# Optimization experiments

Hardware: AMD Instinct MI355X
Metric: run time of the kernel (lower is better)

## Reference

```python
import jax, jax.numpy as jnp
import numpy as np

RAY_START, RAY_END = 2.25, 3.3
DEPTH_RES, N_IMPORTANCE = 48, 48
BOX_WARP = 1.0
PLANE_AXES = jnp.array([[[1.,0.,0.],[0.,1.,0.],[0.,0.,1.]],
                        [[1.,0.,0.],[0.,0.,1.],[0.,1.,0.]],
                        [[0.,0.,1.],[1.,0.,0.],[0.,1.,0.]]], jnp.float32)


def grid_sample_bilinear(feat, gx, gy):
    # feat [B,C,H,W]; gx,gy [B,M] in [-1,1]; bilinear, zeros padding, align_corners=False
    B, C, H, W = feat.shape
    x = (gx + 1.0) * (W * 0.5) - 0.5
    y = (gy + 1.0) * (H * 0.5) - 0.5
    x0 = jnp.floor(x); y0 = jnp.floor(y)
    wx = (x - x0)[:, None, :]; wy = (y - y0)[:, None, :]
    x0i = x0.astype(jnp.int32); y0i = y0.astype(jnp.int32)
    flat = feat.reshape(B, C, H * W)
    def gather(xi, yi):
        valid = ((xi >= 0) & (xi < W) & (yi >= 0) & (yi < H)).astype(feat.dtype)
        idx = jnp.clip(yi, 0, H - 1) * W + jnp.clip(xi, 0, W - 1)
        v = jnp.take_along_axis(flat, jnp.broadcast_to(idx[:, None, :], (B, C, idx.shape[-1])), axis=2)
        return v * valid[:, None, :]
    v00 = gather(x0i, y0i); v10 = gather(x0i + 1, y0i)
    v01 = gather(x0i, y0i + 1); v11 = gather(x0i + 1, y0i + 1)
    return (v00 * (1 - wx) * (1 - wy) + v10 * wx * (1 - wy)
            + v01 * (1 - wx) * wy + v11 * wx * wy)  # [B,C,M]


def sample_from_planes(planes_feat, coords):
    # planes_feat [N,3,C,H,W], coords [N,M,3] -> [N,3,M,C]
    N, P, C, H, W = planes_feat.shape
    M = coords.shape[1]
    c = (2.0 / BOX_WARP) * coords
    inv = jnp.linalg.inv(PLANE_AXES)  # [P,3,3]
    proj = jnp.einsum('nmi,pij->npmj', c, inv)[..., :2]
    out = grid_sample_bilinear(planes_feat.reshape(N * P, C, H, W),
                               proj[..., 0].reshape(N * P, M),
                               proj[..., 1].reshape(N * P, M))
    return out.reshape(N, P, C, M).transpose(0, 1, 3, 2)


def decode(feats, w1, b1, w2, b2):
    # OSGDecoder: mean over planes, Linear->softplus->Linear
    x = feats.mean(axis=1)
    h = jax.nn.softplus(x @ w1 + b1)
    o = h @ w2 + b2
    sigma = o[..., :1]
    rgb = jax.nn.sigmoid(o[..., 1:]) * (1 + 2 * 0.001) - 0.001
    return rgb, sigma


def ray_march(colors, densities, depths, color_bg=None):
    # MipRayMarcher2 with softplus density clamp and BG compositing via final transmittance
    deltas = depths[:, :, 1:] - depths[:, :, :-1]
    colors_mid = 0.5 * (colors[:, :, :-1] + colors[:, :, 1:])
    densities_mid = jax.nn.softplus(0.5 * (densities[:, :, :-1] + densities[:, :, 1:]) - 1.0)
    depths_mid = 0.5 * (depths[:, :, :-1] + depths[:, :, 1:])
    alpha = 1.0 - jnp.exp(-densities_mid * deltas)
    alpha_shifted = jnp.concatenate([jnp.ones_like(alpha[:, :, :1]), 1 - alpha + 1e-10], axis=2)
    T = jnp.cumprod(alpha_shifted, axis=2)
    weights = alpha * T[:, :, :-1]
    comp_rgb = (weights * colors_mid).sum(axis=2)
    weight_total = weights.sum(axis=2)
    comp_depth = jnp.nan_to_num((weights * depths_mid).sum(axis=2) / weight_total, nan=float('inf'))
    comp_depth = jnp.clip(comp_depth, depths.min(), depths.max())
    bg_trans = T[:, :, -1]  # [B,R,1]
    if color_bg is not None:
        comp_rgb = comp_rgb + bg_trans * color_bg
    comp_rgb = comp_rgb * 2.0 - 1.0
    return comp_rgb, comp_depth, weights, alpha, bg_trans


def sample_pdf(bins, weights, n_importance, eps=1e-5):
    # inverse-CDF importance sampling (deterministic midpoint u)
    nw = weights.shape[-1]
    weights = weights + eps
    pdf = weights / weights.sum(axis=-1, keepdims=True)
    cdf = jnp.concatenate([jnp.zeros_like(pdf[:, :1]), jnp.cumsum(pdf, axis=-1)], axis=-1)
    u = (jnp.arange(n_importance, dtype=cdf.dtype) + 0.5) / n_importance
    u = jnp.broadcast_to(u, (cdf.shape[0], n_importance))
    inds = jax.vmap(lambda c, uu: jnp.searchsorted(c, uu, side='right'))(cdf, u)
    below = jnp.clip(inds - 1, 0, nw)
    above = jnp.clip(inds, 0, nw)
    cdf_b = jnp.take_along_axis(cdf, below, axis=-1)
    cdf_a = jnp.take_along_axis(cdf, above, axis=-1)
    bins_b = jnp.take_along_axis(bins, below, axis=-1)
    bins_a = jnp.take_along_axis(bins, above, axis=-1)
    denom = jnp.where(cdf_a - cdf_b < eps, 1.0, cdf_a - cdf_b)
    return bins_b + (u - cdf_b) / denom * (bins_a - bins_b)


def sample_importance(z_vals, weights, n_importance):
    B, R, S, _ = z_vals.shape
    z = z_vals.reshape(B * R, S)
    w = weights.reshape(B * R, -1) + 0.01
    wp = jnp.pad(w, ((0, 0), (1, 1)), constant_values=-np.inf)
    w = jnp.maximum(wp[:, :-1], wp[:, 1:])      # max_pool1d(k=2,s=1,p=1)
    w = 0.5 * (w[:, :-1] + w[:, 1:]) + 0.01     # avg_pool1d(k=2,s=1)
    z_mid = 0.5 * (z[:, :-1] + z[:, 1:])
    z_fine = sample_pdf(z_mid, w[:, 1:-1], n_importance)
    return jax.lax.stop_gradient(z_fine).reshape(B, R, n_importance, 1)


def unify_samples(d1, c1, s1, d2, c2, s2):
    depths = jnp.concatenate([d1, d2], axis=2)
    colors = jnp.concatenate([c1, c2], axis=2)
    dens = jnp.concatenate([s1, s2], axis=2)
    idx = jnp.argsort(depths, axis=2)
    depths = jnp.take_along_axis(depths, idx, axis=2)
    colors = jnp.take_along_axis(colors, jnp.broadcast_to(idx, colors.shape), axis=2)
    dens = jnp.take_along_axis(dens, idx, axis=2)
    return depths, colors, dens


def sample_stratified(B, R, dtype):
    S = DEPTH_RES
    delta = (RAY_END - RAY_START) / (S - 1)
    d = jnp.linspace(RAY_START, RAY_END, S, dtype=dtype).reshape(1, 1, S, 1) + 0.5 * delta
    return jnp.broadcast_to(d, (B, R, S, 1))


def setup_inputs() -> dict:
    key = jax.random.key(0)
    ks = jax.random.split(key, 10)
    B, R, C, H = 4, 4096, 32, 256
    planes = 0.1 * jax.random.normal(ks[0], (B, 3, C, H, H), jnp.float32)
    ray_origins = jnp.array([0.0, 0.0, 2.7]) + 0.03 * jax.random.normal(ks[1], (B, R, 3), jnp.float32)
    uv = jax.random.uniform(ks[2], (B, R, 2), jnp.float32, -0.4, 0.4)
    d = jnp.concatenate([uv, -jnp.ones((B, R, 1), jnp.float32)], axis=-1)
    ray_directions = d / jnp.linalg.norm(d, axis=-1, keepdims=True)
    z_bg = jax.random.normal(ks[3], (B, 64), jnp.float32)
    dec_w1 = jax.random.normal(ks[4], (C, 64), jnp.float32) / np.sqrt(C)
    dec_b1 = jnp.zeros((64,), jnp.float32)
    dec_w2 = jax.random.normal(ks[5], (64, 33), jnp.float32) / 8.0
    dec_b2 = jnp.zeros((33,), jnp.float32)
    bg_w1 = jax.random.normal(ks[6], (67, 64), jnp.float32) / np.sqrt(67)
    bg_b1 = jnp.zeros((64,), jnp.float32)
    bg_w2 = jax.random.normal(ks[7], (64, 32), jnp.float32) / 8.0
    bg_b2 = jnp.zeros((32,), jnp.float32)
    return dict(planes=planes, ray_origins=ray_origins, ray_directions=ray_directions, z_bg=z_bg,
                dec_w1=dec_w1, dec_b1=dec_b1, dec_w2=dec_w2, dec_b2=dec_b2,
                bg_w1=bg_w1, bg_b1=bg_b1, bg_w2=bg_w2, bg_b2=bg_b2)


def reference(planes, ray_origins, ray_directions, z_bg, dec_w1, dec_b1, dec_w2, dec_b2,
              bg_w1, bg_b1, bg_w2, bg_b2):
    B, R, _ = ray_origins.shape
    S = DEPTH_RES
    depths_coarse = sample_stratified(B, R, planes.dtype)
    coords = (ray_origins[:, :, None, :] + depths_coarse * ray_directions[:, :, None, :]).reshape(B, -1, 3)
    feats = sample_from_planes(planes, coords)
    rgb_c, sig_c = decode(feats, dec_w1, dec_b1, dec_w2, dec_b2)
    rgb_c = rgb_c.reshape(B, R, S, -1)
    sig_c = sig_c.reshape(B, R, S, 1)
    # Ball background feature: MLP on [dir, z_bg]
    z = jnp.broadcast_to(z_bg[:, None, :], (B, R, z_bg.shape[-1]))
    hb = jax.nn.softplus(jnp.concatenate([ray_directions, z], axis=-1) @ bg_w1 + bg_b1)
    color_bg = jax.nn.sigmoid(hb @ bg_w2 + bg_b2)  # [B,R,32]
    _, _, w_coarse, _, _ = ray_march(rgb_c, sig_c, depths_coarse)
    depths_fine = sample_importance(depths_coarse, w_coarse, N_IMPORTANCE)
    coords_f = (ray_origins[:, :, None, :] + depths_fine * ray_directions[:, :, None, :]).reshape(B, -1, 3)
    feats_f = sample_from_planes(planes, coords_f)
    rgb_f, sig_f = decode(feats_f, dec_w1, dec_b1, dec_w2, dec_b2)
    rgb_f = rgb_f.reshape(B, R, N_IMPORTANCE, -1)
    sig_f = sig_f.reshape(B, R, N_IMPORTANCE, 1)
    depths_all, rgb_all, sig_all = unify_samples(depths_coarse, rgb_c, sig_c, depths_fine, rgb_f, sig_f)
    rgb_final, depth_final, weights, alpha, bg_T = ray_march(rgb_all, sig_all, depths_all, color_bg)
    return rgb_final, depth_final, weights.sum(axis=2)
```

## Files before the change

### kernel.cpp

```cpp
#include <hip/hip_runtime.h>
#include <hip/hip_bf16.h>
#include <math.h>

#define NB 4
#define NR 4096
#define NC 32
#define NH 256
#define NW 256
#define NS 48
#define NRAYS (NB*NR)
#define NSAMP (NRAYS*NS)

__device__ __forceinline__ float coarse_depth(int i) {
    const float DELTA = 1.05f / 47.f;
    return 2.25f + i * DELTA + 0.5f * DELTA;
}
__device__ __forceinline__ float zmid_c(int i) {
    return 0.5f * (coarse_depth(i) + coarse_depth(i + 1));
}
__device__ __forceinline__ float softplus_f(float x) {
    return fmaxf(x, 0.f) + __logf(1.f + __expf(-fabsf(x)));
}
__device__ __forceinline__ float sigmoid_f(float x) {
    return __frcp_rn(1.f + __expf(-x));
}

__global__ __launch_bounds__(256) void k_transpose(const float* __restrict__ in,
                                                   float* __restrict__ out) {
    __shared__ float tile[32][65];
    int bp = blockIdx.x >> 10;
    int t0 = (blockIdx.x & 1023) * 64;
    const float* src = in + (size_t)bp * NC * NH * NW;
    float* dst = out + (size_t)bp * NH * NW * NC;
    int px = threadIdx.x & 63;
    int c0 = threadIdx.x >> 6;
    #pragma unroll
    for (int cc = 0; cc < 32; cc += 4)
        tile[cc + c0][px] = src[(size_t)(cc + c0) * NH * NW + t0 + px];
    __syncthreads();
    int c = threadIdx.x & 31;
    int p0 = threadIdx.x >> 5;
    #pragma unroll
    for (int pp = 0; pp < 64; pp += 8)
        dst[(size_t)(t0 + pp + p0) * NC + c] = tile[c][pp + p0];
}

__global__ __launch_bounds__(64) void k_const(const float* __restrict__ b1,
                                              const float* __restrict__ w2,
                                              const float* __restrict__ b2,
                                              float* __restrict__ const_o) {
    __shared__ float h[64];
    int j = threadIdx.x;
    h[j] = softplus_f(b1[j]);
    __syncthreads();
    if (j < 33) {
        float o = b2[j];
        #pragma unroll 1
        for (int i = 0; i < 64; ++i) o += h[i] * w2[i * 33 + j];
        const_o[j] = (j == 0) ? o : sigmoid_f(o) * 1.002f - 0.001f;
    }
}

template<bool FINE>
__global__ __launch_bounds__(256) void k_sample_decode(
    const float* __restrict__ planes_t,
    const float* __restrict__ origins,
    const float* __restrict__ dirs,
    const float* __restrict__ dfine,
    const float* __restrict__ w1, const float* __restrict__ b1,
    const float* __restrict__ w2, const float* __restrict__ b2,
    const float* __restrict__ const_o,
    float* __restrict__ rgb_out, float* __restrict__ sig_out)
{
    __shared__ float xbuf[256][33];
    __shared__ float w1t[64][32];
    __shared__ float w2p[64][36];
    __shared__ float b1s[64];
    __shared__ float b2s[36];
    __shared__ float cbuf[36];

    for (int i = threadIdx.x; i < 2048; i += 256) {
        int j = i >> 5, c = i & 31;
        w1t[j][c] = w1[c * 64 + j];
    }
    for (int i = threadIdx.x; i < 64 * 36; i += 256) {
        int j = i / 36, kx = i - j * 36;
        w2p[j][kx] = (kx < 33) ? w2[j * 33 + kx] : 0.f;
    }
    if (threadIdx.x < 64) b1s[threadIdx.x] = b1[threadIdx.x];
    if (threadIdx.x < 36) {
        b2s[threadIdx.x]  = (threadIdx.x < 33) ? b2[threadIdx.x] : 0.f;
        cbuf[threadIdx.x] = (threadIdx.x < 33) ? const_o[threadIdx.x] : 0.f;
    }

    int lane  = threadIdx.x & 63;
    int wbase = threadIdx.x & 192;
    int s0    = blockIdx.x * 256 + wbase;

    int s   = s0 + lane;
    int ray = s / NS;
    int kk  = s - ray * NS;
    float t = FINE ? dfine[s] : coarse_depth(kk);
    float ox = origins[ray*3+0], oy = origins[ray*3+1], oz = origins[ray*3+2];
    float ddx = dirs[ray*3+0],   ddy = dirs[ray*3+1],   ddz = dirs[ray*3+2];
    float cx = 2.f * (ox + t * ddx);
    float cy = 2.f * (oy + t * ddy);
    float cz = 2.f * (oz + t * ddz);
    int bi = ray >> 12;
    int   m_base[3];
    float m_q[3][4];
    #pragma unroll
    for (int p = 0; p < 3; ++p) {
        float gx = (p == 2) ? cz : cx;
        float gy = (p == 0) ? cy : ((p == 1) ? cz : cx);
        float fx = (gx + 1.f) * 128.f - 0.5f;
        float fy = (gy + 1.f) * 128.f - 0.5f;
        float x0f = floorf(fx), y0f = floorf(fy);
        float wx = fx - x0f, wy = fy - y0f;
        int x0 = (int)x0f, y0 = (int)y0f;
        if (x0 >= -1 && x0 <= 255 && y0 >= -1 && y0 <= 255) {
            float wxm = 1.f - wx, wym = 1.f - wy;
            float q00 = wxm*wym, q10 = wx*wym, q01 = wxm*wy, q11 = wx*wy;
            if (!(x0 >= 0   && y0 >= 0))   q00 = 0.f;
            if (!(x0 <= 254 && y0 >= 0))   q10 = 0.f;
            if (!(x0 >= 0   && y0 <= 254)) q01 = 0.f;
            if (!(x0 <= 254 && y0 <= 254)) q11 = 0.f;
            m_base[p] = (bi*3 + p) * (NH*NW*NC) + (y0*NW + x0)*NC;
            m_q[p][0] = q00; m_q[p][1] = q10; m_q[p][2] = q01; m_q[p][3] = q11;
        } else {
            m_base[p] = -1;
            m_q[p][0] = m_q[p][1] = m_q[p][2] = m_q[p][3] = 0.f;
        }
    }

    int ch   = lane & 31;
    int half = lane >> 5;
    #pragma unroll 1
    for (int i = 0; i < 64; i += 2) {
        int src = i + half;
        float acc = 0.f;
        #pragma unroll
        for (int p = 0; p < 3; ++p) {
            int   bse = __shfl(m_base[p], src);
            float q00 = __shfl(m_q[p][0], src);
            float q10 = __shfl(m_q[p][1], src);
            float q01 = __shfl(m_q[p][2], src);
            float q11 = __shfl(m_q[p][3], src);
            if (bse >= 0) {
                const float* ptr = planes_t + (size_t)bse + ch;
                acc += q00 * ptr[0]    + q10 * ptr[32]
                     + q01 * ptr[8192] + q11 * ptr[8224];
            }
        }
        xbuf[wbase + i + half][ch] = acc * (1.f / 3.f);
    }
    __syncthreads();

    bool empty = (m_base[0] < 0) & (m_base[1] < 0) & (m_base[2] < 0);
    float sig;
    if (!empty) {
        float x[32];
        #pragma unroll
        for (int c = 0; c < 32; ++c) x[c] = xbuf[threadIdx.x][c];
        float o[36];
        #pragma unroll
        for (int k2 = 0; k2 < 36; ++k2) o[k2] = b2s[k2];
        #pragma unroll 1
        for (int j = 0; j < 64; ++j) {
            float a = b1s[j];
            #pragma unroll
            for (int c = 0; c < 32; ++c) a += x[c] * w1t[j][c];
            float h = softplus_f(a);
            #pragma unroll
            for (int k2 = 0; k2 < 36; ++k2) o[k2] += h * w2p[j][k2];
        }
        sig = o[0];
        #pragma unroll
        for (int c = 0; c < 32; ++c)
            xbuf[threadIdx.x][c] = sigmoid_f(o[1 + c]) * 1.002f - 0.001f;
    } else {
        sig = cbuf[0];
        #pragma unroll
        for (int c = 0; c < 32; ++c) xbuf[threadIdx.x][c] = cbuf[1 + c];
    }
    sig_out[s] = sig;
    __syncthreads();

    #pragma unroll 1
    for (int i = 0; i < 64; i += 2) {
        int r = wbase + i + half;
        rgb_out[(size_t)(blockIdx.x * 256 + r) * 32 + ch] = xbuf[r][ch];
    }
}

__global__ __launch_bounds__(256) void k_importance(const float* __restrict__ sig,
                                                    float* __restrict__ dfine) {
    int ray = blockIdx.x * 256 + threadIdx.x;
    const float* sp = sig + (size_t)ray * NS;
    float w[47];
    float T = 1.f;
    float sprev = sp[0];
    #pragma unroll
    for (int i = 0; i < 47; ++i) {
        float scur = sp[i + 1];
        float dens = softplus_f(0.5f * (sprev + scur) - 1.f);
        float delta = coarse_depth(i + 1) - coarse_depth(i);
        float alpha = 1.f - __expf(-dens * delta);
        w[i] = alpha * T + 0.01f;
        T *= (1.f - alpha + 1e-10f);
        sprev = scur;
    }
    float p[45];
    float sum = 0.f;
    #pragma unroll
    for (int i = 1; i <= 45; ++i) {
        float nwi  = fmaxf(w[i - 1], w[i]);
        float nwi1 = fmaxf(w[i], w[i + 1]);
        float wb = 0.5f * (nwi + nwi1) + 0.01f;
        float v = wb + 1e-5f;
        p[i - 1] = v;
        sum += v;
    }
    int k = 0;
    float cdf_lo = 0.f;
    #pragma unroll
    for (int i = 0; i < 45; ++i) {
        float cdf_hi = cdf_lo + p[i] / sum;
        float bb = zmid_c(i), ba = zmid_c(i + 1);
        float denom = cdf_hi - cdf_lo;
        if (denom < 1e-5f) denom = 1.f;
        while (k < 48) {
            float u = (k + 0.5f) / 48.f;
            if (u < cdf_hi) {
                dfine[(size_t)ray * NS + k] = bb + (u - cdf_lo) / denom * (ba - bb);
                ++k;
            } else break;
        }
        cdf_lo = cdf_hi;
    }
    while (k < 48) {
        dfine[(size_t)ray * NS + k] = zmid_c(45);
        ++k;
    }
}

__global__ __launch_bounds__(256) void k_final(
    const float* __restrict__ sig_c, const float* __restrict__ rgb_c,
    const float* __restrict__ sig_f, const float* __restrict__ rgb_f,
    const float* __restrict__ dfine,
    const float* __restrict__ dirs, const float* __restrict__ z_bg,
    const float* __restrict__ bw1, const float* __restrict__ bb1,
    const float* __restrict__ bw2, const float* __restrict__ bb2,
    float* __restrict__ out_rgb, float* __restrict__ out_dep,
    float* __restrict__ out_wt)
{
    __shared__ float s_d[4][96];
    __shared__ float s_sig[4][96];
    __shared__ int   s_src[4][96];
    __shared__ float s_fine[4][48];
    __shared__ float s_w[4][96];
    __shared__ float s_g[4][96];
    __shared__ float s_h[4][64];
    __shared__ float s_zb[64];
    int lane = threadIdx.x & 63;
    int wv = threadIdx.x >> 6;
    int ray = blockIdx.x * 4 + wv;
    int bi = (blockIdx.x * 4) >> 12;
    if (threadIdx.x < 64) s_zb[threadIdx.x] = z_bg[bi * 64 + threadIdx.x];
    if (lane < 48) s_fine[wv][lane] = dfine[(size_t)ray * NS + lane];
    __syncthreads();

    if (lane < 48) {
        float cd = coarse_depth(lane);
        int lo = 0, hi = 48;
        while (lo < hi) { int mid = (lo + hi) >> 1;
            if (s_fine[wv][mid] < cd) lo = mid + 1; else hi = mid; }
        int rc = lane + lo;
        s_d[wv][rc] = cd;
        s_sig[wv][rc] = sig_c[(size_t)ray * NS + lane];
        s_src[wv][rc] = lane;
        float f = s_fine[wv][lane];
        lo = 0; hi = 48;
        while (lo < hi) { int mid = (lo + hi) >> 1;
            if (coarse_depth(mid) <= f) lo = mid + 1; else hi = mid; }
        int rf = lane + lo;
        s_d[wv][rf] = f;
        s_sig[wv][rf] = sig_f[(size_t)ray * NS + lane];
        s_src[wv][rf] = 48 + lane;
    }
    float ddx = dirs[ray*3+0], ddy = dirs[ray*3+1], ddz = dirs[ray*3+2];
    __syncthreads();

    float alpha0 = 0.f, alpha1 = 0.f, a0 = 1.f, a1 = 1.f;
    float dm0 = 0.f, dm1 = 0.f;
    if (lane < 48) {
        int i0 = 2 * lane, i1 = i0 + 1;
        float d0 = s_d[wv][i0], sA = s_sig[wv][i0];
        float d1 = s_d[wv][i1], sB = s_sig[wv][i1];
        {
            float dens = softplus_f(0.5f * (sA + sB) - 1.f);
            alpha0 = 1.f - __expf(-dens * (d1 - d0));
            a0 = 1.f - alpha0 + 1e-10f;
            dm0 = 0.5f * (d0 + d1);
        }
        if (i1 < 95) {
            float d2 = s_d[wv][i1 + 1], sC = s_sig[wv][i1 + 1];
            float dens = softplus_f(0.5f * (sB + sC) - 1.f);
            alpha1 = 1.f - __expf(-dens * (d2 - d1));
            a1 = 1.f - alpha1 + 1e-10f;
            dm1 = 0.5f * (d1 + d2);
        }
    }
    float P = a0 * a1;
    #pragma unroll
    for (int off = 1; off < 64; off <<= 1) {
        float t = __shfl_up(P, off);
        if (lane >= off) P *= t;
    }
    float T_all = __shfl(P, 63);
    float E = __shfl_up(P, 1);
    if (lane == 0) E = 1.f;
    float w0 = alpha0 * E;
    float w1 = alpha1 * (E * a0);
    float sw = w0 + w1;
    float sd = w0 * dm0 + w1 * dm1;
    #pragma unroll
    for (int off = 32; off; off >>= 1) {
        sw += __shfl_xor(sw, off);
        sd += __shfl_xor(sd, off);
    }
    if (lane < 48) {
        s_w[wv][2 * lane] = w0;
        s_w[wv][2 * lane + 1] = w1;
    }
    __syncthreads();
    {
        int i = lane;
        float wm = (i > 0) ? s_w[wv][i - 1] : 0.f;
        s_g[wv][i] = 0.5f * (wm + s_w[wv][i]);
        int i2 = lane + 64;
        if (lane < 32)
            s_g[wv][i2] = 0.5f * (s_w[wv][i2 - 1] + s_w[wv][i2]);
    }

    float a = bb1[lane] + ddx * bw1[lane] + ddy * bw1[64 + lane] + ddz * bw1[128 + lane];
    #pragma unroll 1
    for (int i = 0; i < 64; ++i) a += s_zb[i] * bw1[(3 + i) * 64 + lane];
    s_h[wv][lane] = softplus_f(a);
    __syncthreads();
    int c = lane & 31;
    float ob = bb2[c];
    #pragma unroll 1
    for (int j = 0; j < 64; ++j) ob += s_h[wv][j] * bw2[j * 32 + c];
    float bgc = sigmoid_f(ob);

    int h = lane >> 5;
    size_t rbase = (size_t)ray * NS * 32;
    const float* b0p = rgb_c + rbase;
    const float* b1p = rgb_f + rbase - (size_t)48 * 32;
    float acc = 0.f;
    #pragma unroll 4
    for (int i = h; i < 96; i += 2) {
        int src = s_src[wv][i];
        const float* cp = ((src < 48) ? b0p : b1p) + (size_t)src * 32;
        acc += s_g[wv][i] * cp[c];
    }
    acc += __shfl_xor(acc, 32);

    float rgbv = (acc + T_all * bgc) * 2.f - 1.f;
    float dep = sd / sw;
    if (!(dep == dep)) dep = INFINITY;
    dep = fminf(fmaxf(dep, coarse_depth(0)), coarse_depth(47));
    if (lane < 32) out_rgb[(size_t)ray * 32 + c] = rgbv;
    if (lane == 0) { out_dep[ray] = dep; out_wt[ray] = sw; }
}

extern "C" void kernel_launch(void* const* d_in, const int* in_sizes, int n_in,
                              void* d_out, int out_size, void* d_ws, size_t ws_size,
                              hipStream_t stream) {
    (void)in_sizes; (void)n_in; (void)out_size; (void)ws_size;
    const float* planes  = (const float*)d_in[0];
    const float* origins = (const float*)d_in[1];
    const float* dirs    = (const float*)d_in[2];
    const float* z_bg    = (const float*)d_in[3];
    const float* dw1     = (const float*)d_in[4];
    const float* db1     = (const float*)d_in[5];
    const float* dw2     = (const float*)d_in[6];
    const float* db2     = (const float*)d_in[7];
    const float* bw1     = (const float*)d_in[8];
    const float* bb1     = (const float*)d_in[9];
    const float* bw2     = (const float*)d_in[10];
    const float* bb2     = (const float*)d_in[11];

    char* ws = (char*)d_ws;
    size_t off = 0;
    float* sig_c    = (float*)(ws + off); off += (size_t)NSAMP * 4;
    float* sig_f    = (float*)(ws + off); off += (size_t)NSAMP * 4;
    float* dfine    = (float*)(ws + off); off += (size_t)NSAMP * 4;
    float* const_o  = (float*)(ws + off); off += 4096;
    float* planes_t = (float*)(ws + off); off += (size_t)NB * 3 * NH * NW * NC * 4;
    float* rgb_c    = (float*)(ws + off); off += (size_t)NSAMP * 32 * 4;
    float* rgb_f    = (float*)(ws + off); off += (size_t)NSAMP * 32 * 4;

    float* out_rgb = (float*)d_out;
    float* out_dep = out_rgb + (size_t)NRAYS * 32;
    float* out_wt  = out_dep + NRAYS;

    k_const<<<dim3(1), dim3(64), 0, stream>>>(db1, dw2, db2, const_o);
    k_transpose<<<dim3(NB * 3 * 1024), dim3(256), 0, stream>>>(planes, planes_t);
    k_sample_decode<false><<<dim3(NSAMP / 256), dim3(256), 0, stream>>>(
        planes_t, origins, dirs, (const float*)nullptr,
        dw1, db1, dw2, db2, const_o, rgb_c, sig_c);
    k_importance<<<dim3(NRAYS / 256), dim3(256), 0, stream>>>(sig_c, dfine);
    k_sample_decode<true><<<dim3(NSAMP / 256), dim3(256), 0, stream>>>(
        planes_t, origins, dirs, dfine,
        dw1, db1, dw2, db2, const_o, rgb_f, sig_f);
    k_final<<<dim3(NRAYS / 4), dim3(256), 0, stream>>>(
        sig_c, rgb_c, sig_f, rgb_f, dfine, dirs, z_bg,
        bw1, bb1, bw2, bb2, out_rgb, out_dep, out_wt);
}
```

Measured before the change: 893.7 us.

## Split fused sample-decode kernel into separate gather and MLP kernels

Splits the combined plane-sampling and decoder kernel into a gather kernel that writes averaged features to global memory and a separate MLP kernel. The MLP kernel reads those features back with float4 loads, takes weights from global memory (pre-transposed once by a prep kernel) instead of LDS, and overwrites the features with rgb in place. The aim is to decouple the memory-bound gather from the compute-bound MLP so each gets better occupancy and register allocation. In exchange it adds an extra round trip of the full feature tensor through global memory and drops the skip path for samples that fall outside all planes.

```diff
diff --git a/kernel.cpp b/kernel.cpp
--- a/kernel.cpp
+++ b/kernel.cpp
@@ -45,54 +45,28 @@
         dst[(size_t)(t0 + pp + p0) * NC + c] = tile[c][pp + p0];
 }
 
-__global__ __launch_bounds__(64) void k_const(const float* __restrict__ b1,
+__global__ __launch_bounds__(256) void k_prep(const float* __restrict__ w1,
                                               const float* __restrict__ w2,
-                                              const float* __restrict__ b2,
-                                              float* __restrict__ const_o) {
-    __shared__ float h[64];
-    int j = threadIdx.x;
-    h[j] = softplus_f(b1[j]);
-    __syncthreads();
-    if (j < 33) {
-        float o = b2[j];
-        #pragma unroll 1
-        for (int i = 0; i < 64; ++i) o += h[i] * w2[i * 33 + j];
-        const_o[j] = (j == 0) ? o : sigmoid_f(o) * 1.002f - 0.001f;
+                                              float* __restrict__ w1t,
+                                              float* __restrict__ w2p) {
+    for (int i = threadIdx.x; i < 2048; i += 256) {
+        int j = i >> 5, c = i & 31;
+        w1t[j * 32 + c] = w1[c * 64 + j];
+    }
+    for (int i = threadIdx.x; i < 64 * 36; i += 256) {
+        int j = i / 36, kx = i - j * 36;
+        w2p[i] = (kx < 33) ? w2[j * 33 + kx] : 0.f;
     }
 }
 
 template<bool FINE>
-__global__ __launch_bounds__(256) void k_sample_decode(
+__global__ __launch_bounds__(256) void k_gather(
     const float* __restrict__ planes_t,
     const float* __restrict__ origins,
     const float* __restrict__ dirs,
     const float* __restrict__ dfine,
-    const float* __restrict__ w1, const float* __restrict__ b1,
-    const float* __restrict__ w2, const float* __restrict__ b2,
-    const float* __restrict__ const_o,
-    float* __restrict__ rgb_out, float* __restrict__ sig_out)
+    float* __restrict__ feats_out)
 {
-    __shared__ float xbuf[256][33];
-    __shared__ float w1t[64][32];
-    __shared__ float w2p[64][36];
-    __shared__ float b1s[64];
-    __shared__ float b2s[36];
-    __shared__ float cbuf[36];
-
-    for (int i = threadIdx.x; i < 2048; i += 256) {
-        int j = i >> 5, c = i & 31;
-        w1t[j][c] = w1[c * 64 + j];
-    }
-    for (int i = threadIdx.x; i < 64 * 36; i += 256) {
-        int j = i / 36, kx = i - j * 36;
-        w2p[j][kx] = (kx < 33) ? w2[j * 33 + kx] : 0.f;
-    }
-    if (threadIdx.x < 64) b1s[threadIdx.x] = b1[threadIdx.x];
-    if (threadIdx.x < 36) {
-        b2s[threadIdx.x]  = (threadIdx.x < 33) ? b2[threadIdx.x] : 0.f;
-        cbuf[threadIdx.x] = (threadIdx.x < 33) ? const_o[threadIdx.x] : 0.f;
-    }
-
     int lane  = threadIdx.x & 63;
     int wbase = threadIdx.x & 192;
     int s0    = blockIdx.x * 256 + wbase;
@@ -152,44 +126,47 @@
                      + q01 * ptr[8192] + q11 * ptr[8224];
             }
         }
-        xbuf[wbase + i + half][ch] = acc * (1.f / 3.f);
-    }
-    __syncthreads();
-
-    bool empty = (m_base[0] < 0) & (m_base[1] < 0) & (m_base[2] < 0);
-    float sig;
-    if (!empty) {
-        float x[32];
+        feats_out[(size_t)(s0 + i + half) * 32 + ch] = acc * (1.f / 3.f);
+    }
+}
+
+__global__ __launch_bounds__(256) void k_mlp(
+    const float* __restrict__ w1t,
+    const float* __restrict__ b1,
+    const float* __restrict__ w2p,
+    const float* __restrict__ b2,
+    float* __restrict__ rgb_io,
+    float* __restrict__ sig_out)
+{
+    int s = blockIdx.x * 256 + threadIdx.x;
+    float* base = rgb_io + (size_t)s * 32;
+    float x[32];
+    #pragma unroll
+    for (int i = 0; i < 8; ++i) {
+        float4 v = ((const float4*)base)[i];
+        x[4*i+0] = v.x; x[4*i+1] = v.y; x[4*i+2] = v.z; x[4*i+3] = v.w;
+    }
+    float o[33];
+    #pragma unroll
+    for (int k2 = 0; k2 < 33; ++k2) o[k2] = b2[k2];
+    #pragma unroll 4
+    for (int j = 0; j < 64; ++j) {
+        float a = b1[j];
         #pragma unroll
-        for (int c = 0; c < 32; ++c) x[c] = xbuf[threadIdx.x][c];
-        float o[36];
+        for (int c = 0; c < 32; ++c) a += x[c] * w1t[j * 32 + c];
+        float h = softplus_f(a);
         #pragma unroll
-        for (int k2 = 0; k2 < 36; ++k2) o[k2] = b2s[k2];
-        #pragma unroll 1
-        for (int j = 0; j < 64; ++j) {
-            float a = b1s[j];
-            #pragma unroll
-            for (int c = 0; c < 32; ++c) a += x[c] * w1t[j][c];
-            float h = softplus_f(a);
-            #pragma unroll
-            for (int k2 = 0; k2 < 36; ++k2) o[k2] += h * w2p[j][k2];
-        }
-        sig = o[0];
-        #pragma unroll
-        for (int c = 0; c < 32; ++c)
-            xbuf[threadIdx.x][c] = sigmoid_f(o[1 + c]) * 1.002f - 0.001f;
-    } else {
-        sig = cbuf[0];
-        #pragma unroll
-        for (int c = 0; c < 32; ++c) xbuf[threadIdx.x][c] = cbuf[1 + c];
-    }
-    sig_out[s] = sig;
-    __syncthreads();
-
-    #pragma unroll 1
-    for (int i = 0; i < 64; i += 2) {
-        int r = wbase + i + half;
-        rgb_out[(size_t)(blockIdx.x * 256 + r) * 32 + ch] = xbuf[r][ch];
+        for (int k2 = 0; k2 < 33; ++k2) o[k2] += h * w2p[j * 36 + k2];
+    }
+    sig_out[s] = o[0];
+    #pragma unroll
+    for (int i = 0; i < 8; ++i) {
+        float4 r;
+        r.x = sigmoid_f(o[1 + 4*i + 0]) * 1.002f - 0.001f;
+        r.y = sigmoid_f(o[1 + 4*i + 1]) * 1.002f - 0.001f;
+        r.z = sigmoid_f(o[1 + 4*i + 2]) * 1.002f - 0.001f;
+        r.w = sigmoid_f(o[1 + 4*i + 3]) * 1.002f - 0.001f;
+        ((float4*)base)[i] = r;
     }
 }
 
@@ -397,7 +374,8 @@
     float* sig_c    = (float*)(ws + off); off += (size_t)NSAMP * 4;
     float* sig_f    = (float*)(ws + off); off += (size_t)NSAMP * 4;
     float* dfine    = (float*)(ws + off); off += (size_t)NSAMP * 4;
-    float* const_o  = (float*)(ws + off); off += 4096;
+    float* w1t      = (float*)(ws + off); off += 64 * 32 * 4;
+    float* w2p      = (float*)(ws + off); off += 64 * 36 * 4;
     float* planes_t = (float*)(ws + off); off += (size_t)NB * 3 * NH * NW * NC * 4;
     float* rgb_c    = (float*)(ws + off); off += (size_t)NSAMP * 32 * 4;
     float* rgb_f    = (float*)(ws + off); off += (size_t)NSAMP * 32 * 4;
@@ -406,15 +384,17 @@
     float* out_dep = out_rgb + (size_t)NRAYS * 32;
     float* out_wt  = out_dep + NRAYS;
 
-    k_const<<<dim3(1), dim3(64), 0, stream>>>(db1, dw2, db2, const_o);
+    k_prep<<<dim3(1), dim3(256), 0, stream>>>(dw1, dw2, w1t, w2p);
     k_transpose<<<dim3(NB * 3 * 1024), dim3(256), 0, stream>>>(planes, planes_t);
-    k_sample_decode<false><<<dim3(NSAMP / 256), dim3(256), 0, stream>>>(
-        planes_t, origins, dirs, (const float*)nullptr,
-        dw1, db1, dw2, db2, const_o, rgb_c, sig_c);
+    k_gather<false><<<dim3(NSAMP / 256), dim3(256), 0, stream>>>(
+        planes_t, origins, dirs, (const float*)nullptr, rgb_c);
+    k_mlp<<<dim3(NSAMP / 256), dim3(256), 0, stream>>>(
+        w1t, db1, w2p, db2, rgb_c, sig_c);
     k_importance<<<dim3(NRAYS / 256), dim3(256), 0, stream>>>(sig_c, dfine);
-    k_sample_decode<true><<<dim3(NSAMP / 256), dim3(256), 0, stream>>>(
-        planes_t, origins, dirs, dfine,
-        dw1, db1, dw2, db2, const_o, rgb_f, sig_f);
+    k_gather<true><<<dim3(NSAMP / 256), dim3(256), 0, stream>>>(
+        planes_t, origins, dirs, dfine, rgb_f);
+    k_mlp<<<dim3(NSAMP / 256), dim3(256), 0, stream>>>(
+        w1t, db1, w2p, db2, rgb_f, sig_f);
     k_final<<<dim3(NRAYS / 4), dim3(256), 0, stream>>>(
         sig_c, rgb_c, sig_f, rgb_f, dfine, dirs, z_bg,
         bw1, bb1, bw2, bb2, out_rgb, out_dep, out_wt);
```

Measured after the change: 772.1 us. -13.6%, faster.
